# Kernel optimization log

Hardware: AMD Instinct MI355X
Metric: run time of the kernel (lower is better)

The kernel has to match this reference:

```python
import jax, jax.numpy as jnp
import numpy as np

NB_TS = 4          # module-level global nb_timestep in the original code
EMBED = 512
SQRT_DIM = float(np.sqrt(EMBED))


def _conv(x, w, b=None):
    # torch Conv2d(kernel=3, stride=1, padding=1), NCHW / OIHW
    y = jax.lax.conv_general_dilated(x, w, (1, 1), ((1, 1), (1, 1)),
                                     dimension_numbers=('NCHW', 'OIHW', 'NCHW'))
    if b is not None:
        y = y + b[None, :, None, None]
    return y


def setup_inputs() -> dict:
    B, C, H, W = 8, 512, 16, 16
    TXT = 256
    key = jax.random.key(0)
    ks = iter(jax.random.split(key, 40))

    def nrm(shape, s=0.02):
        return jax.random.normal(next(ks), shape, jnp.float32) * s

    inp = {
        'x':   jax.random.normal(next(ks), (B, C, H, W), jnp.float32),
        'txt': jax.random.normal(next(ks), (B, 1, TXT), jnp.float32),
        # attention convs
        'Wa_w': nrm((C, C, 3, 3)), 'Wa_b': nrm((C,)),
        'Ua_w': nrm((C, C, 3, 3)), 'Ua_b': nrm((C,)),
        'Va_w': nrm((1, C, 3, 3)),
        # gate convs
        'Wi_w': nrm((C, C, 3, 3)), 'Wi_b': nrm((C,)),
        'Ui_w': nrm((C, C, 3, 3)), 'Ui_b': nrm((C,)),
        'Wf_w': nrm((C, C, 3, 3)), 'Wf_b': nrm((C,)),
        'Uf_w': nrm((C, C, 3, 3)), 'Uf_b': nrm((C,)),
        'Wc_w': nrm((C, C, 3, 3)), 'Wc_b': nrm((C,)),
        'Uc_w': nrm((C, C, 3, 3)), 'Uc_b': nrm((C,)),
        'Wo_w': nrm((C, C, 3, 3)), 'Wo_b': nrm((C,)),
        'Uo_w': nrm((C, C, 3, 3)), 'Uo_b': nrm((C,)),
        # text attention linears (torch Linear weight layout [out, in])
        'WQ': nrm((EMBED * H * W, TXT)),
        'WK': nrm((EMBED, 1)),
        'WV': nrm((EMBED, 1)),
        'Wsum_w': nrm((1, EMBED)), 'Wsum_b': nrm((1,)),
    }
    return inp


def reference(x, txt, Wa_w, Wa_b, Ua_w, Ua_b, Va_w,
              Wi_w, Wi_b, Ui_w, Ui_b, Wf_w, Wf_b, Uf_w, Uf_b,
              Wc_w, Wc_b, Uc_w, Uc_b, Wo_w, Wo_b, Uo_w, Uo_b,
              WQ, WK, WV, Wsum_w, Wsum_b):
    B, _, Hs, Ws = x.shape
    txt2 = txt.reshape(txt.shape[0], txt.shape[2])  # [B, 256]
    h = x
    c = x
    # Q is timestep-invariant; hoist out of the loop (same math)
    Q = (txt2 @ WQ.T).reshape(B, Hs, Ws, EMBED)  # [B,H,W,E]
    for _ in range(NB_TS):
        Z = _conv(jnp.tanh(_conv(h, Wa_w, Wa_b) + _conv(x, Ua_w, Ua_b)), Va_w)  # [B,1,H,W]
        A1 = jax.nn.softmax(Z, axis=1)          # softmax over channel dim of size 1 (faithful)
        Ap = jnp.transpose(A1, (0, 2, 3, 1))    # [B,H,W,1]
        K = Ap @ WK.T                            # [B,H,W,E]
        V = Ap @ WV.T                            # [B,H,W,E]
        scores = jnp.sum(Q * K, axis=3, keepdims=True) / SQRT_DIM  # [B,H,W,1]
        attn = jax.nn.softmax(scores, axis=1)    # torch softmax(dim=1) -> over H axis
        # repeat(...,embed_dim)*V is just a broadcast multiply
        A2 = (attn * V) @ Wsum_w.T + Wsum_b      # [B,H,W,1]
        A2 = jnp.transpose(A2, (0, 3, 1, 2))     # [B,1,H,W]
        myA = A1 + A2
        AM = myA * x
        i = jax.nn.sigmoid(_conv(AM, Wi_w, Wi_b) + _conv(h, Ui_w, Ui_b))
        f = jax.nn.sigmoid(_conv(AM, Wf_w, Wf_b) + _conv(h, Uf_w, Uf_b))
        o = jax.nn.sigmoid(_conv(AM, Wo_w, Wo_b) + _conv(h, Uo_w, Uo_b))
        g = jnp.tanh(_conv(AM, Wc_w, Wc_b) + _conv(h, Uc_w, Uc_b))
        c = g * i + f * c
        h = jnp.tanh(c) * o
    return h
```

## Files before the change

kernel.cpp:

```cpp
#include <hip/hip_runtime.h>

typedef unsigned short u16;
typedef __attribute__((ext_vector_type(8))) _Float16 f16x8;
typedef __attribute__((ext_vector_type(4))) float f32x4;
typedef __attribute__((ext_vector_type(4))) int i32x4;
typedef __attribute__((ext_vector_type(4))) unsigned short us4;

__device__ __forceinline__ u16 f2h(float f) {
  _Float16 h = (_Float16)f;
  return __builtin_bit_cast(unsigned short, h);
}
__device__ __forceinline__ float sigm(float v) { return 1.0f / (1.0f + __expf(-v)); }
__device__ __forceinline__ float tanh_(float v) {
  float t = __expf(-2.0f * fabsf(v));
  float r = (1.0f - t) / (1.0f + t);
  return v >= 0.0f ? r : -r;
}

typedef const __attribute__((address_space(1))) unsigned int* gas_t;
typedef __attribute__((address_space(3))) unsigned int* las_t;
__device__ __forceinline__ void gl16(const u16* g, u16* l) {
  __builtin_amdgcn_global_load_lds((gas_t)g, (las_t)l, 16, 0, 0);
}

__global__ __launch_bounds__(256, 4) void prep_big(
    const float* __restrict__ WQ, const float* __restrict__ WK,
    const float* __restrict__ txt, const float* __restrict__ WV,
    const float* __restrict__ Wsw, const float* __restrict__ Wsb,
    const float* __restrict__ wi, const float* __restrict__ wf,
    const float* __restrict__ wo, const float* __restrict__ wc,
    const float* __restrict__ ui, const float* __restrict__ uf,
    const float* __restrict__ uo, const float* __restrict__ uc,
    u16* __restrict__ dstW, u16* __restrict__ dstU,
    float* __restrict__ scores, float* __restrict__ sb) {
  __shared__ float red[4][8];
  __shared__ float red2[4];
  int tid = threadIdx.x;
  if (blockIdx.x < 2048) {
    int p = blockIdx.x & 255;
    int es = blockIdx.x >> 8;
    int t4 = tid & 63, eg = tid >> 6;
    const f32x4* base = (const f32x4*)WQ + ((size_t)p * 512 + es * 64 + eg * 16) * 64 + t4;
    f32x4 va[16];
#pragma unroll
    for (int i = 0; i < 16; ++i) va[i] = base[i * 64];
    f32x4 wkq[4];
    const f32x4* wkp = (const f32x4*)(WK + es * 64 + eg * 16);
#pragma unroll
    for (int i = 0; i < 4; ++i) wkq[i] = wkp[i];
    f32x4 m4 = {0.f, 0.f, 0.f, 0.f};
#pragma unroll
    for (int i = 0; i < 4; ++i)
#pragma unroll
      for (int e = 0; e < 4; ++e) m4 += va[i * 4 + e] * wkq[i][e];
    float v[8];
    const f32x4* txp = (const f32x4*)txt;
#pragma unroll
    for (int b = 0; b < 8; ++b) {
      f32x4 tx = txp[b * 64 + t4];
      v[b] = m4[0] * tx[0] + m4[1] * tx[1] + m4[2] * tx[2] + m4[3] * tx[3];
    }
#pragma unroll
    for (int off = 32; off; off >>= 1)
#pragma unroll
      for (int b = 0; b < 8; ++b) v[b] += __shfl_down(v[b], off, 64);
    if (t4 == 0)
#pragma unroll
      for (int b = 0; b < 8; ++b) red[eg][b] = v[b];
    __syncthreads();
    if (tid < 8) {
      float sv = red[0][tid] + red[1][tid] + red[2][tid] + red[3][tid];
      atomicAdd(&scores[tid * 256 + p], sv * 0.044194173824159216f);
    }
    if (blockIdx.x == 0) {
      float vv = WV[tid] * Wsw[tid] + WV[tid + 256] * Wsw[tid + 256];
#pragma unroll
      for (int off = 32; off; off >>= 1) vv += __shfl_down(vv, off, 64);
      if (t4 == 0) red2[eg] = vv;
      __syncthreads();
      if (tid == 0) {
        sb[0] = red2[0] + red2[1] + red2[2] + red2[3];
        sb[1] = Wsb[0];
      }
    }
    return;
  }
  int sbid = blockIdx.x - 2048;
  int set = sbid >> 9;
  int chgrp = (sbid >> 4) & 31;
  int chunk = sbid & 15;
  int q = tid & 3, gch = tid >> 2;
  int gate = gch >> 4, chrow = gch & 15;
  int ch = chgrp * 16 + chrow;
  const float* s;
  if (set == 0) s = gate == 0 ? wi : gate == 1 ? wf : gate == 2 ? wo : wc;
  else          s = gate == 0 ? ui : gate == 1 ? uf : gate == 2 ? uo : uc;
  const f32x4* src = (const f32x4*)(s + (size_t)(ch * 512 + chunk * 32) * 9) + q * 18;
  f32x4 va[18];
#pragma unroll
  for (int i = 0; i < 18; ++i) va[i] = src[i];
  u16* dst = (set == 0 ? dstW : dstU) + (size_t)(chgrp * 16 + chunk) * 18432
             + (size_t)(gate * 64 + q * 16 + chrow) * 8;
#pragma unroll
  for (int k9 = 0; k9 < 9; ++k9) {
    i32x4 wv;
#pragma unroll
    for (int w = 0; w < 4; ++w) {
      int i0 = (2 * w) * 9 + k9, i1 = (2 * w + 1) * 9 + k9;
      unsigned lo = f2h(va[i0 >> 2][i0 & 3]);
      unsigned hi = f2h(va[i1 >> 2][i1 & 3]);
      wv[w] = (int)(lo | (hi << 16));
    }
    *(i32x4*)(dst + k9 * 2048) = wv;
  }
}

__global__ void prep_inputs(const float* __restrict__ x, const float* __restrict__ scores,
                            const float* __restrict__ sb,
                            u16* __restrict__ AM, u16* __restrict__ H0) {
  __shared__ float sc[16];
  int idx = blockIdx.x * 256 + threadIdx.x;
  int ch = idx & 511, p = (idx >> 9) & 255, b = idx >> 17;
  int w = p & 15, h = p >> 4;
  if (threadIdx.x < 16) sc[threadIdx.x] = scores[b * 256 + threadIdx.x * 16 + w];
  __syncthreads();
  float s = sb[0], b0 = sb[1];
  float mx = -1e30f;
#pragma unroll
  for (int hh = 0; hh < 16; ++hh) mx = fmaxf(mx, sc[hh]);
  float den = 0.f, my = 0.f;
#pragma unroll
  for (int hh = 0; hh < 16; ++hh) {
    float e = __expf(sc[hh] - mx);
    den += e;
    if (hh == h) my = e;
  }
  float coef = 1.0f + b0 + s * my / den;
  float xv = x[(size_t)(b * 512 + ch) * 256 + p];
  AM[idx] = f2h(coef * xv);
  H0[idx] = f2h(xv);
}

template <int MODE>
__launch_bounds__(512, 2)
__global__ void conv4(const u16* __restrict__ inA, const u16* __restrict__ inH,
                      const u16* __restrict__ wW, const u16* __restrict__ wU,
                      const float* __restrict__ bWi, const float* __restrict__ bUi,
                      const float* __restrict__ bWf, const float* __restrict__ bUf,
                      const float* __restrict__ bWo, const float* __restrict__ bUo,
                      const float* __restrict__ bWc, const float* __restrict__ bUc,
                      float* __restrict__ G, const float* __restrict__ c_src,
                      float* __restrict__ c_dst, u16* __restrict__ h_out,
                      float* __restrict__ out) {
  __shared__ __align__(16) u16 Alds[2][9 * 4 * 64 * 8];
  __shared__ __align__(16) u16 Blds[2][18 * 18 * 32];
  const int tid = threadIdx.x;
  const int chgrp = blockIdx.x & 31;
  const int b = blockIdx.x >> 5;
  const int wave = tid >> 6, lane = tid & 63;
  const int row = lane & 15, quad = lane >> 4;
  const int NCH = (MODE == 0) ? 32 : 16;

  {
    i32x4 z = {0, 0, 0, 0};
    i32x4* bz = (i32x4*)&Blds[0][0];
#pragma unroll
    for (int i = 0; i < 6; ++i) {
      int k = tid + 512 * i;
      if (k < 2592) bz[k] = z;
    }
  }
  __syncthreads();

  const u16* wsrcW = wW + (size_t)chgrp * 294912;
  const u16* wsrcU = wU + (size_t)chgrp * 294912;
  const u16* isrcA = inA + (size_t)b * 131072;
  const u16* isrcH = inH + (size_t)b * 131072;

  auto stage = [&](int k, int bb) {
    const u16* gw;
    const u16* gi;
    if (MODE == 0 && k < 16) { gw = wsrcW + k * 18432; gi = isrcA + k * 32; }
    else                     { gw = wsrcU + (k & 15) * 18432; gi = isrcH + (k & 15) * 32; }
    u16* Ab = &Alds[bb][0];
#pragma unroll
    for (int i = 0; i < 5; ++i) {
      int idx = i * 8 + wave;
      if (idx < 36) gl16(gw + (idx * 64 + lane) * 8, &Ab[idx * 512]);
    }
    u16* Bb = &Blds[bb][0];
    int xi = lane >> 2;
    int qsrc = (lane & 3) ^ (((xi + 1) >> 2) & 3);
#pragma unroll
    for (int j = 0; j < 2; ++j) {
      int gy = wave + j * 8;
      gl16(gi + (size_t)(gy * 16 + xi) * 512 + qsrc * 8, &Bb[(gy + 1) * 576 + 32]);
    }
  };

  f32x4 acc[4][2];
#pragma unroll
  for (int m = 0; m < 4; ++m)
#pragma unroll
    for (int n = 0; n < 2; ++n) acc[m][n] = (f32x4){0.f, 0.f, 0.f, 0.f};

  const int ch0 = chgrp * 16 + quad * 4;
  float* gptr = G + (size_t)blockIdx.x * 16384 + wave * 2048 + lane * 4;

  stage(0, 0);
  __syncthreads();
  int bb = 0;

#pragma unroll 1
  for (int k = 0; k < NCH; ++k) {
    if (k + 1 < NCH) stage(k + 1, bb ^ 1);
    const u16* Ab = &Alds[bb][0];
    const u16* Bb = &Blds[bb][0];
#pragma unroll
    for (int kx = 0; kx < 3; ++kx) {
      int xx = row + kx;
      int qs = quad ^ ((xx >> 2) & 3);
      f16x8 bfr[4];
#pragma unroll
      for (int jj = 0; jj < 4; ++jj)
        bfr[jj] = *(const f16x8*)(&Bb[(wave * 2 + jj) * 576 + xx * 32 + qs * 8]);
#pragma unroll
      for (int ky = 0; ky < 3; ++ky) {
#pragma unroll
        for (int m = 0; m < 4; ++m) {
          f16x8 af = *(const f16x8*)(&Ab[((ky * 3 + kx) * 4 + m) * 512 + lane * 8]);
#pragma unroll
          for (int n = 0; n < 2; ++n)
            acc[m][n] = __builtin_amdgcn_mfma_f32_16x16x32_f16(af, bfr[n + ky], acc[m][n], 0, 0, 0);
        }
      }
    }
    if constexpr (MODE == 0) {
      if (k == 15) {
#pragma unroll
        for (int m = 0; m < 4; ++m) {
          const float* bw = m == 0 ? bWi : m == 1 ? bWf : m == 2 ? bWo : bWc;
          const float* bu = m == 0 ? bUi : m == 1 ? bUf : m == 2 ? bUo : bUc;
          f32x4 bias;
#pragma unroll
          for (int r = 0; r < 4; ++r) bias[r] = bw[ch0 + r] + bu[ch0 + r];
#pragma unroll
          for (int n = 0; n < 2; ++n) {
            acc[m][n] = acc[m][n] + bias;
            *(f32x4*)(gptr + (m * 2 + n) * 256) = acc[m][n];
          }
        }
      }
    }
    __syncthreads();
    bb ^= 1;
  }

#pragma unroll
  for (int n = 0; n < 2; ++n) {
    const int p = (wave * 2 + n) * 16 + row;
    f32x4 zi = acc[0][n], zf = acc[1][n], zo = acc[2][n], zg = acc[3][n];
    if constexpr (MODE != 0) {
      zi = zi + *(const f32x4*)(gptr + (0 + n) * 256);
      zf = zf + *(const f32x4*)(gptr + (2 + n) * 256);
      zo = zo + *(const f32x4*)(gptr + (4 + n) * 256);
      zg = zg + *(const f32x4*)(gptr + (6 + n) * 256);
    }
    f32x4 cold;
#pragma unroll
    for (int r = 0; r < 4; ++r)
      cold[r] = c_src[(size_t)(b * 512 + ch0 + r) * 256 + p];
    f32x4 cnew, hv;
#pragma unroll
    for (int r = 0; r < 4; ++r) {
      float iv = sigm(zi[r]);
      float fv = sigm(zf[r]);
      float ov = sigm(zo[r]);
      float gv = tanh_(zg[r]);
      float cn = fmaf(gv, iv, fv * cold[r]);
      cnew[r] = cn;
      hv[r] = tanh_(cn) * ov;
    }
    if constexpr (MODE != 2) {
#pragma unroll
      for (int r = 0; r < 4; ++r)
        c_dst[(size_t)(b * 512 + ch0 + r) * 256 + p] = cnew[r];
      us4 hb;
      hb[0] = f2h(hv[0]); hb[1] = f2h(hv[1]);
      hb[2] = f2h(hv[2]); hb[3] = f2h(hv[3]);
      *(us4*)(h_out + (size_t)b * 131072 + (size_t)p * 512 + ch0) = hb;
    } else {
#pragma unroll
      for (int r = 0; r < 4; ++r)
        out[(size_t)(b * 512 + ch0 + r) * 256 + p] = hv[r];
    }
  }
}

extern "C" void kernel_launch(void* const* d_in, const int* in_sizes, int n_in,
                              void* d_out, int out_size, void* d_ws, size_t ws_size,
                              hipStream_t stream) {
  const float* x    = (const float*)d_in[0];
  const float* txt  = (const float*)d_in[1];
  const float* Wi_w = (const float*)d_in[7];
  const float* Wi_b = (const float*)d_in[8];
  const float* Ui_w = (const float*)d_in[9];
  const float* Ui_b = (const float*)d_in[10];
  const float* Wf_w = (const float*)d_in[11];
  const float* Wf_b = (const float*)d_in[12];
  const float* Uf_w = (const float*)d_in[13];
  const float* Uf_b = (const float*)d_in[14];
  const float* Wc_w = (const float*)d_in[15];
  const float* Wc_b = (const float*)d_in[16];
  const float* Uc_w = (const float*)d_in[17];
  const float* Uc_b = (const float*)d_in[18];
  const float* Wo_w = (const float*)d_in[19];
  const float* Wo_b = (const float*)d_in[20];
  const float* Uo_w = (const float*)d_in[21];
  const float* Uo_b = (const float*)d_in[22];
  const float* WQ   = (const float*)d_in[23];
  const float* WK   = (const float*)d_in[24];
  const float* WV   = (const float*)d_in[25];
  const float* Wsw  = (const float*)d_in[26];
  const float* Wsb  = (const float*)d_in[27];
  (void)in_sizes; (void)n_in; (void)ws_size;

  char* ws = (char*)d_ws;
  size_t off = 0;
  auto carve = [&](size_t n) {
    char* p = ws + off;
    off += (n + 255) & ~(size_t)255;
    return p;
  };
  u16* WswzW    = (u16*)carve(18874368);
  u16* WswzU    = (u16*)carve(18874368);
  u16* AM       = (u16*)carve(2097152);
  u16* H0       = (u16*)carve(2097152);
  u16* H1       = (u16*)carve(2097152);
  float* G      = (float*)carve(16777216);
  float* C      = (float*)carve(4194304);
  float* scores = (float*)carve(8192);
  float* sb     = (float*)carve(256);

  hipMemsetAsync(scores, 0, 8192, stream);

  prep_big<<<3072, 256, 0, stream>>>(WQ, WK, txt, WV, Wsw, Wsb,
                                     Wi_w, Wf_w, Wo_w, Wc_w,
                                     Ui_w, Uf_w, Uo_w, Uc_w,
                                     WswzW, WswzU, scores, sb);
  prep_inputs<<<4096, 256, 0, stream>>>(x, scores, sb, AM, H0);

  conv4<0><<<256, 512, 0, stream>>>(AM, H0, WswzW, WswzU,
                                    Wi_b, Ui_b, Wf_b, Uf_b, Wo_b, Uo_b, Wc_b, Uc_b,
                                    G, x, C, H1, nullptr);
  conv4<1><<<256, 512, 0, stream>>>(nullptr, H1, nullptr, WswzU,
                                    nullptr, nullptr, nullptr, nullptr,
                                    nullptr, nullptr, nullptr, nullptr,
                                    G, C, C, H0, nullptr);
  conv4<1><<<256, 512, 0, stream>>>(nullptr, H0, nullptr, WswzU,
                                    nullptr, nullptr, nullptr, nullptr,
                                    nullptr, nullptr, nullptr, nullptr,
                                    G, C, C, H1, nullptr);
  conv4<2><<<256, 512, 0, stream>>>(nullptr, H1, nullptr, WswzU,
                                    nullptr, nullptr, nullptr, nullptr,
                                    nullptr, nullptr, nullptr, nullptr,
                                    G, C, nullptr, nullptr, (float*)d_out);
}
```

Measured before the change: 516.2 us.

## Retile conv waves to 2 gates by 4 rows and split prep kernel

The conv kernel's per-wave MFMA tile changes from 4 gates by 2 pixel rows to 2 gates by 4 pixel rows. This lets B fragments be reused across more MFMAs and A fragments be loaded up front. Because each pixel's gates now sit in two different waves, the epilogue passes the o/g accumulators through LDS with an extra barrier before the LSTM cell update. Separately, the fused prep kernel is split into a scores kernel and a weight-swizzle kernel, and sched_barriers are added so loads issue before compute.

Result: no change. 508.2 us (-1.6%).

```diff
diff --git a/kernel.cpp b/kernel.cpp
--- a/kernel.cpp
+++ b/kernel.cpp
@@ -23,69 +23,71 @@
   __builtin_amdgcn_global_load_lds((gas_t)g, (las_t)l, 16, 0, 0);
 }
 
-__global__ __launch_bounds__(256, 4) void prep_big(
+__global__ __launch_bounds__(256, 4) void prep_scores(
     const float* __restrict__ WQ, const float* __restrict__ WK,
     const float* __restrict__ txt, const float* __restrict__ WV,
     const float* __restrict__ Wsw, const float* __restrict__ Wsb,
+    float* __restrict__ scores, float* __restrict__ sb) {
+  __shared__ float red[4][8];
+  __shared__ float red2[4];
+  int tid = threadIdx.x;
+  int p = blockIdx.x & 255;
+  int es = blockIdx.x >> 8;
+  int t4 = tid & 63, eg = tid >> 6;
+  const f32x4* base = (const f32x4*)WQ + ((size_t)p * 512 + es * 64 + eg * 16) * 64 + t4;
+  f32x4 va[16];
+#pragma unroll
+  for (int i = 0; i < 16; ++i) va[i] = base[i * 64];
+  f32x4 wkq[4];
+  const f32x4* wkp = (const f32x4*)(WK + es * 64 + eg * 16);
+#pragma unroll
+  for (int i = 0; i < 4; ++i) wkq[i] = wkp[i];
+  __builtin_amdgcn_sched_barrier(0);
+  f32x4 m4 = {0.f, 0.f, 0.f, 0.f};
+#pragma unroll
+  for (int i = 0; i < 4; ++i)
+#pragma unroll
+    for (int e = 0; e < 4; ++e) m4 += va[i * 4 + e] * wkq[i][e];
+  float v[8];
+  const f32x4* txp = (const f32x4*)txt;
+#pragma unroll
+  for (int b = 0; b < 8; ++b) {
+    f32x4 tx = txp[b * 64 + t4];
+    v[b] = m4[0] * tx[0] + m4[1] * tx[1] + m4[2] * tx[2] + m4[3] * tx[3];
+  }
+#pragma unroll
+  for (int off = 32; off; off >>= 1)
+#pragma unroll
+    for (int b = 0; b < 8; ++b) v[b] += __shfl_down(v[b], off, 64);
+  if (t4 == 0)
+#pragma unroll
+    for (int b = 0; b < 8; ++b) red[eg][b] = v[b];
+  __syncthreads();
+  if (tid < 8) {
+    float sv = red[0][tid] + red[1][tid] + red[2][tid] + red[3][tid];
+    atomicAdd(&scores[tid * 256 + p], sv * 0.044194173824159216f);
+  }
+  if (blockIdx.x == 0) {
+    float vv = WV[tid] * Wsw[tid] + WV[tid + 256] * Wsw[tid + 256];
+#pragma unroll
+    for (int off = 32; off; off >>= 1) vv += __shfl_down(vv, off, 64);
+    if (t4 == 0) red2[eg] = vv;
+    __syncthreads();
+    if (tid == 0) {
+      sb[0] = red2[0] + red2[1] + red2[2] + red2[3];
+      sb[1] = Wsb[0];
+    }
+  }
+}
+
+__global__ __launch_bounds__(256, 4) void prep_swz(
     const float* __restrict__ wi, const float* __restrict__ wf,
     const float* __restrict__ wo, const float* __restrict__ wc,
     const float* __restrict__ ui, const float* __restrict__ uf,
     const float* __restrict__ uo, const float* __restrict__ uc,
-    u16* __restrict__ dstW, u16* __restrict__ dstU,
-    float* __restrict__ scores, float* __restrict__ sb) {
-  __shared__ float red[4][8];
-  __shared__ float red2[4];
+    u16* __restrict__ dstW, u16* __restrict__ dstU) {
   int tid = threadIdx.x;
-  if (blockIdx.x < 2048) {
-    int p = blockIdx.x & 255;
-    int es = blockIdx.x >> 8;
-    int t4 = tid & 63, eg = tid >> 6;
-    const f32x4* base = (const f32x4*)WQ + ((size_t)p * 512 + es * 64 + eg * 16) * 64 + t4;
-    f32x4 va[16];
-#pragma unroll
-    for (int i = 0; i < 16; ++i) va[i] = base[i * 64];
-    f32x4 wkq[4];
-    const f32x4* wkp = (const f32x4*)(WK + es * 64 + eg * 16);
-#pragma unroll
-    for (int i = 0; i < 4; ++i) wkq[i] = wkp[i];
-    f32x4 m4 = {0.f, 0.f, 0.f, 0.f};
-#pragma unroll
-    for (int i = 0; i < 4; ++i)
-#pragma unroll
-      for (int e = 0; e < 4; ++e) m4 += va[i * 4 + e] * wkq[i][e];
-    float v[8];
-    const f32x4* txp = (const f32x4*)txt;
-#pragma unroll
-    for (int b = 0; b < 8; ++b) {
-      f32x4 tx = txp[b * 64 + t4];
-      v[b] = m4[0] * tx[0] + m4[1] * tx[1] + m4[2] * tx[2] + m4[3] * tx[3];
-    }
-#pragma unroll
-    for (int off = 32; off; off >>= 1)
-#pragma unroll
-      for (int b = 0; b < 8; ++b) v[b] += __shfl_down(v[b], off, 64);
-    if (t4 == 0)
-#pragma unroll
-      for (int b = 0; b < 8; ++b) red[eg][b] = v[b];
-    __syncthreads();
-    if (tid < 8) {
-      float sv = red[0][tid] + red[1][tid] + red[2][tid] + red[3][tid];
-      atomicAdd(&scores[tid * 256 + p], sv * 0.044194173824159216f);
-    }
-    if (blockIdx.x == 0) {
-      float vv = WV[tid] * Wsw[tid] + WV[tid + 256] * Wsw[tid + 256];
-#pragma unroll
-      for (int off = 32; off; off >>= 1) vv += __shfl_down(vv, off, 64);
-      if (t4 == 0) red2[eg] = vv;
-      __syncthreads();
-      if (tid == 0) {
-        sb[0] = red2[0] + red2[1] + red2[2] + red2[3];
-        sb[1] = Wsb[0];
-      }
-    }
-    return;
-  }
-  int sbid = blockIdx.x - 2048;
+  int sbid = blockIdx.x;
   int set = sbid >> 9;
   int chgrp = (sbid >> 4) & 31;
   int chunk = sbid & 15;
@@ -99,6 +101,7 @@
   f32x4 va[18];
 #pragma unroll
   for (int i = 0; i < 18; ++i) va[i] = src[i];
+  __builtin_amdgcn_sched_barrier(0);
   u16* dst = (set == 0 ? dstW : dstU) + (size_t)(chgrp * 16 + chunk) * 18432
              + (size_t)(gate * 64 + q * 16 + chrow) * 8;
 #pragma unroll
@@ -159,6 +162,7 @@
   const int b = blockIdx.x >> 5;
   const int wave = tid >> 6, lane = tid & 63;
   const int row = lane & 15, quad = lane >> 4;
+  const int nw = wave & 3, mw = wave >> 2;
   const int NCH = (MODE == 0) ? 32 : 16;
 
   {
@@ -198,11 +202,11 @@
     }
   };
 
-  f32x4 acc[4][2];
-#pragma unroll
-  for (int m = 0; m < 4; ++m)
-#pragma unroll
-    for (int n = 0; n < 2; ++n) acc[m][n] = (f32x4){0.f, 0.f, 0.f, 0.f};
+  f32x4 acc[2][4];
+#pragma unroll
+  for (int m = 0; m < 2; ++m)
+#pragma unroll
+    for (int jj = 0; jj < 4; ++jj) acc[m][jj] = (f32x4){0.f, 0.f, 0.f, 0.f};
 
   const int ch0 = chgrp * 16 + quad * 4;
   float* gptr = G + (size_t)blockIdx.x * 16384 + wave * 2048 + lane * 4;
@@ -220,34 +224,39 @@
     for (int kx = 0; kx < 3; ++kx) {
       int xx = row + kx;
       int qs = quad ^ ((xx >> 2) & 3);
-      f16x8 bfr[4];
-#pragma unroll
-      for (int jj = 0; jj < 4; ++jj)
-        bfr[jj] = *(const f16x8*)(&Bb[(wave * 2 + jj) * 576 + xx * 32 + qs * 8]);
-#pragma unroll
-      for (int ky = 0; ky < 3; ++ky) {
-#pragma unroll
-        for (int m = 0; m < 4; ++m) {
-          f16x8 af = *(const f16x8*)(&Ab[((ky * 3 + kx) * 4 + m) * 512 + lane * 8]);
-#pragma unroll
-          for (int n = 0; n < 2; ++n)
-            acc[m][n] = __builtin_amdgcn_mfma_f32_16x16x32_f16(af, bfr[n + ky], acc[m][n], 0, 0, 0);
-        }
-      }
+      f16x8 bfr[6];
+#pragma unroll
+      for (int rr = 0; rr < 6; ++rr)
+        bfr[rr] = *(const f16x8*)(&Bb[(4 * nw + rr) * 576 + xx * 32 + qs * 8]);
+      f16x8 afr[6];
+#pragma unroll
+      for (int ky = 0; ky < 3; ++ky)
+#pragma unroll
+        for (int m = 0; m < 2; ++m)
+          afr[ky * 2 + m] = *(const f16x8*)(&Ab[((ky * 3 + kx) * 4 + 2 * mw + m) * 512 + lane * 8]);
+#pragma unroll
+      for (int ky = 0; ky < 3; ++ky)
+#pragma unroll
+        for (int m = 0; m < 2; ++m)
+#pragma unroll
+          for (int jj = 0; jj < 4; ++jj)
+            acc[m][jj] = __builtin_amdgcn_mfma_f32_16x16x32_f16(afr[ky * 2 + m], bfr[jj + ky],
+                                                                acc[m][jj], 0, 0, 0);
     }
     if constexpr (MODE == 0) {
       if (k == 15) {
 #pragma unroll
-        for (int m = 0; m < 4; ++m) {
-          const float* bw = m == 0 ? bWi : m == 1 ? bWf : m == 2 ? bWo : bWc;
-          const float* bu = m == 0 ? bUi : m == 1 ? bUf : m == 2 ? bUo : bUc;
+        for (int m = 0; m < 2; ++m) {
+          int g = 2 * mw + m;
+          const float* bw = g == 0 ? bWi : g == 1 ? bWf : g == 2 ? bWo : bWc;
+          const float* bu = g == 0 ? bUi : g == 1 ? bUf : g == 2 ? bUo : bUc;
           f32x4 bias;
 #pragma unroll
           for (int r = 0; r < 4; ++r) bias[r] = bw[ch0 + r] + bu[ch0 + r];
 #pragma unroll
-          for (int n = 0; n < 2; ++n) {
-            acc[m][n] = acc[m][n] + bias;
-            *(f32x4*)(gptr + (m * 2 + n) * 256) = acc[m][n];
+          for (int jj = 0; jj < 4; ++jj) {
+            acc[m][jj] = acc[m][jj] + bias;
+            *(f32x4*)(gptr + (m * 4 + jj) * 256) = acc[m][jj];
           }
         }
       }
@@ -256,43 +265,57 @@
     bb ^= 1;
   }
 
-#pragma unroll
-  for (int n = 0; n < 2; ++n) {
-    const int p = (wave * 2 + n) * 16 + row;
-    f32x4 zi = acc[0][n], zf = acc[1][n], zo = acc[2][n], zg = acc[3][n];
-    if constexpr (MODE != 0) {
-      zi = zi + *(const f32x4*)(gptr + (0 + n) * 256);
-      zf = zf + *(const f32x4*)(gptr + (2 + n) * 256);
-      zo = zo + *(const f32x4*)(gptr + (4 + n) * 256);
-      zg = zg + *(const f32x4*)(gptr + (6 + n) * 256);
-    }
-    f32x4 cold;
-#pragma unroll
-    for (int r = 0; r < 4; ++r)
-      cold[r] = c_src[(size_t)(b * 512 + ch0 + r) * 256 + p];
-    f32x4 cnew, hv;
-#pragma unroll
-    for (int r = 0; r < 4; ++r) {
-      float iv = sigm(zi[r]);
-      float fv = sigm(zf[r]);
-      float ov = sigm(zo[r]);
-      float gv = tanh_(zg[r]);
-      float cn = fmaf(gv, iv, fv * cold[r]);
-      cnew[r] = cn;
-      hv[r] = tanh_(cn) * ov;
-    }
-    if constexpr (MODE != 2) {
+  if constexpr (MODE != 0) {
+#pragma unroll
+    for (int m = 0; m < 2; ++m)
+#pragma unroll
+      for (int jj = 0; jj < 4; ++jj)
+        acc[m][jj] = acc[m][jj] + *(const f32x4*)(gptr + (m * 4 + jj) * 256);
+  }
+  float* X = (float*)&Blds[0][0];
+  if (mw == 1) {
+#pragma unroll
+    for (int m = 0; m < 2; ++m)
+#pragma unroll
+      for (int jj = 0; jj < 4; ++jj)
+        *(f32x4*)(X + (size_t)(((nw * 2 + m) * 4 + jj) * 256) + lane * 4) = acc[m][jj];
+  }
+  __syncthreads();
+  if (mw == 0) {
+#pragma unroll
+    for (int jj = 0; jj < 4; ++jj) {
+      const int p = (4 * nw + jj) * 16 + row;
+      f32x4 zi = acc[0][jj], zf = acc[1][jj];
+      f32x4 zo = *(const f32x4*)(X + (size_t)(((nw * 2 + 0) * 4 + jj) * 256) + lane * 4);
+      f32x4 zg = *(const f32x4*)(X + (size_t)(((nw * 2 + 1) * 4 + jj) * 256) + lane * 4);
+      f32x4 cold;
 #pragma unroll
       for (int r = 0; r < 4; ++r)
-        c_dst[(size_t)(b * 512 + ch0 + r) * 256 + p] = cnew[r];
-      us4 hb;
-      hb[0] = f2h(hv[0]); hb[1] = f2h(hv[1]);
-      hb[2] = f2h(hv[2]); hb[3] = f2h(hv[3]);
-      *(us4*)(h_out + (size_t)b * 131072 + (size_t)p * 512 + ch0) = hb;
-    } else {
-#pragma unroll
-      for (int r = 0; r < 4; ++r)
-        out[(size_t)(b * 512 + ch0 + r) * 256 + p] = hv[r];
+        cold[r] = c_src[(size_t)(b * 512 + ch0 + r) * 256 + p];
+      f32x4 cnew, hv;
+#pragma unroll
+      for (int r = 0; r < 4; ++r) {
+        float iv = sigm(zi[r]);
+        float fv = sigm(zf[r]);
+        float ov = sigm(zo[r]);
+        float gv = tanh_(zg[r]);
+        float cn = fmaf(gv, iv, fv * cold[r]);
+        cnew[r] = cn;
+        hv[r] = tanh_(cn) * ov;
+      }
+      if constexpr (MODE != 2) {
+#pragma unroll
+        for (int r = 0; r < 4; ++r)
+          c_dst[(size_t)(b * 512 + ch0 + r) * 256 + p] = cnew[r];
+        us4 hb;
+        hb[0] = f2h(hv[0]); hb[1] = f2h(hv[1]);
+        hb[2] = f2h(hv[2]); hb[3] = f2h(hv[3]);
+        *(us4*)(h_out + (size_t)b * 131072 + (size_t)p * 512 + ch0) = hb;
+      } else {
+#pragma unroll
+        for (int r = 0; r < 4; ++r)
+          out[(size_t)(b * 512 + ch0 + r) * 256 + p] = hv[r];
+      }
     }
   }
 }
@@ -344,10 +367,9 @@
 
   hipMemsetAsync(scores, 0, 8192, stream);
 
-  prep_big<<<3072, 256, 0, stream>>>(WQ, WK, txt, WV, Wsw, Wsb,
-                                     Wi_w, Wf_w, Wo_w, Wc_w,
-                                     Ui_w, Uf_w, Uo_w, Uc_w,
-                                     WswzW, WswzU, scores, sb);
+  prep_scores<<<2048, 256, 0, stream>>>(WQ, WK, txt, WV, Wsw, Wsb, scores, sb);
+  prep_swz<<<1024, 256, 0, stream>>>(Wi_w, Wf_w, Wo_w, Wc_w,
+                                     Ui_w, Uf_w, Uo_w, Uc_w, WswzW, WswzU);
   prep_inputs<<<4096, 256, 0, stream>>>(x, scores, sb, AM, H0);
 
   conv4<0><<<256, 512, 0, stream>>>(AM, H0, WswzW, WswzU,
```
